# Kernel optimization log

Measured on AMD Instinct MI355X. Metric: run time of the kernel, lower is better.

## Reference

```python
import jax, jax.numpy as jnp
import numpy as np

EPS = 1e-4  # clamp from module default (0.0001, 1 - 0.0001)


def setup_inputs() -> dict:
    key = jax.random.key(0)
    k1, k2, k3 = jax.random.split(key, 3)
    B, T, C, K = 16, 4096, 512, 3
    x = jax.random.normal(k1, (B, T, C), dtype=jnp.float32)
    # logit_alpha initialized as logit of (0.8, 0.9, 0.98) tiled across channels
    init_alphas = jnp.array([0.8, 0.9, 0.98], dtype=jnp.float32)
    logit_alpha = jnp.broadcast_to(
        (jnp.log(init_alphas) - jnp.log1p(-init_alphas))[:, None], (K, C)
    ).astype(jnp.float32)
    # add small noise so gradients are non-degenerate
    logit_alpha = logit_alpha + 0.01 * jax.random.normal(k2, (K, C), dtype=jnp.float32)
    mix_logits = 0.1 * jax.random.normal(k3, (C, K), dtype=jnp.float32)
    return {"x": x, "logit_alpha": logit_alpha, "mix_logits": mix_logits}


def reference(x, logit_alpha, mix_logits):
    # x: [B,T,C]; logit_alpha: [K,C]; mix_logits: [C,K]
    B, T, C = x.shape
    K = logit_alpha.shape[0]
    a = jnp.clip(jax.nn.sigmoid(logit_alpha), EPS, 1.0 - EPS)  # [K,C]
    b = 1.0 - a

    y0 = jnp.broadcast_to(x[:, 0, None, :], (B, K, C))  # t=0: y = x0 for all K

    def step(y_prev, xt):
        # y_prev: [B,K,C], xt: [B,C]
        y = a * y_prev + b * xt[:, None, :]
        return y, y

    xs = jnp.swapaxes(x[:, 1:, :], 0, 1)  # [T-1,B,C]
    _, ys = jax.lax.scan(step, y0, xs)  # [T-1,B,K,C]
    yk = jnp.concatenate([y0[None], ys], axis=0)  # [T,B,K,C]

    mix = jax.nn.softmax(mix_logits, axis=-1)  # [C,K]
    trend = jnp.einsum('tbkc,ck->tbc', yk, mix)  # [T,B,C]
    return jnp.swapaxes(trend, 0, 1)  # [B,T,C]
```

## Files before the change

### kernel.cpp

```cpp
#include <hip/hip_runtime.h>

#define DEV_INLINE __device__ __forceinline__

constexpr int B = 16, T = 4096, C = 512, K = 3;
constexpr int NC = 64;
constexpr int L  = T / NC;
constexpr int C4 = C / 4;
constexpr float EPS = 1e-4f;


typedef float f4v __attribute__((ext_vector_type(4)));

DEV_INLINE float4 f4mul(float4 a, float4 b) {
  return make_float4(a.x * b.x, a.y * b.y, a.z * b.z, a.w * b.w);
}
DEV_INLINE float4 f4add(float4 a, float4 b) {
  return make_float4(a.x + b.x, a.y + b.y, a.z + b.z, a.w + b.w);
}
DEV_INLINE float4 f4fma(float4 a, float4 b, float4 c) {
  return make_float4(fmaf(a.x, b.x, c.x), fmaf(a.y, b.y, c.y),
                     fmaf(a.z, b.z, c.z), fmaf(a.w, b.w, c.w));
}
DEV_INLINE float4 f4onesub(float4 a) {
  return make_float4(1.f - a.x, 1.f - a.y, 1.f - a.z, 1.f - a.w);
}

DEV_INLINE float sig_clamp(float v) {
  float a = 1.0f / (1.0f + __expf(-v));
  return fminf(fmaxf(a, EPS), 1.0f - EPS);
}
DEV_INLINE float4 sig4(float4 v) {
  return make_float4(sig_clamp(v.x), sig_clamp(v.y), sig_clamp(v.z), sig_clamp(v.w));
}

DEV_INLINE void sm3(float l0, float l1, float l2, float& o0, float& o1, float& o2) {
  float mx = fmaxf(l0, fmaxf(l1, l2));
  float e0 = __expf(l0 - mx), e1 = __expf(l1 - mx), e2 = __expf(l2 - mx);
  float inv = 1.0f / (e0 + e1 + e2);
  o0 = e0 * inv; o1 = e1 * inv; o2 = e2 * inv;
}

DEV_INLINE float4 nt_load(const float4* p) {
  f4v t = __builtin_nontemporal_load(reinterpret_cast<const f4v*>(p));
  float4 r; r.x = t.x; r.y = t.y; r.z = t.z; r.w = t.w; return r;
}

DEV_INLINE void mix4(const float* __restrict__ mix_logits, int c4,
                     float4& m0, float4& m1, float4& m2) {
  const float4* ml = (const float4*)mix_logits;
  const float4 q0 = ml[3 * c4 + 0];
  const float4 q1 = ml[3 * c4 + 1];
  const float4 q2 = ml[3 * c4 + 2];
  sm3(q0.x, q0.y, q0.z, m0.x, m1.x, m2.x);
  sm3(q0.w, q1.x, q1.y, m0.y, m1.y, m2.y);
  sm3(q1.z, q1.w, q2.x, m0.z, m1.z, m2.z);
  sm3(q2.y, q2.z, q2.w, m0.w, m1.w, m2.w);
}

__global__ __launch_bounds__(128) void ema_k1(const float* __restrict__ x,
                                              const float* __restrict__ logit_alpha,
                                              const float* __restrict__ mix_logits,
                                              float* __restrict__ carry_f,
                                              float* __restrict__ out) {
  const int c4 = threadIdx.x;
  const int bi = blockIdx.x;
  const int i  = bi & (NC - 1);

  const float4* la = (const float4*)logit_alpha;
  const float4 a0 = sig4(la[0 * C4 + c4]);
  const float4 a1 = sig4(la[1 * C4 + c4]);
  const float4 a2 = sig4(la[2 * C4 + c4]);
  const float4 b0 = f4onesub(a0), b1 = f4onesub(a1), b2 = f4onesub(a2);

  float4 m0, m1, m2;
  mix4(mix_logits, c4, m0, m1, m2);

  const float4* xb = (const float4*)x + (size_t)bi * L * C4 + c4;
  float4*       ob = (float4*)out     + (size_t)bi * L * C4 + c4;

  float4 y0, y1, y2;
  int jstart;
  if (i == 0) {
    float4 x0 = nt_load(&xb[0]);
    y0 = x0; y1 = x0; y2 = x0;
    ob[0] = f4fma(m0, y0, f4fma(m1, y1, f4mul(m2, y2)));
    jstart = 1;
  } else {
    y0 = make_float4(0.f, 0.f, 0.f, 0.f);
    y1 = y0; y2 = y0;
    jstart = 0;
  }

  #pragma unroll 4
  for (int j = jstart; j < L; ++j) {
    float4 xv = nt_load(&xb[(size_t)j * C4]);
    y0 = f4fma(a0, y0, f4mul(b0, xv));
    y1 = f4fma(a1, y1, f4mul(b1, xv));
    y2 = f4fma(a2, y2, f4mul(b2, xv));
    ob[(size_t)j * C4] = f4fma(m0, y0, f4fma(m1, y1, f4mul(m2, y2)));
  }

  float4* carry = (float4*)carry_f;
  const size_t cb = (size_t)bi * (K * C4) + c4;
  carry[cb + 0 * C4] = y0;
  carry[cb + 1 * C4] = y1;
  carry[cb + 2 * C4] = y2;
}

__global__ __launch_bounds__(128) void ema_k2(const float* __restrict__ logit_alpha,
                                              const float* __restrict__ mix_logits,
                                              const float* __restrict__ carry_f,
                                              float* __restrict__ out) {
  const int c4  = threadIdx.x;
  const int blk = blockIdx.x;
  const int b   = blk / (NC - 1);
  const int i   = blk - b * (NC - 1) + 1;

  const float4* la = (const float4*)logit_alpha;
  const float4 a0 = sig4(la[0 * C4 + c4]);
  const float4 a1 = sig4(la[1 * C4 + c4]);
  const float4 a2 = sig4(la[2 * C4 + c4]);

  float4 m0, m1, m2;
  mix4(mix_logits, c4, m0, m1, m2);

  float4 A0 = a0, A1 = a1, A2 = a2;
  #pragma unroll
  for (int s = 0; s < 6; ++s) { A0 = f4mul(A0, A0); A1 = f4mul(A1, A1); A2 = f4mul(A2, A2); }

  const size_t stride = (size_t)K * C4;
  const float4* cb = (const float4*)carry_f + (size_t)b * NC * stride + c4;
  float4 E0 = cb[0 * C4];
  float4 E1 = cb[1 * C4];
  float4 E2 = cb[2 * C4];
  #pragma unroll 4
  for (int j = 1; j < i; ++j) {
    const float4* cj = cb + (size_t)j * stride;
    E0 = f4fma(A0, E0, cj[0 * C4]);
    E1 = f4fma(A1, E1, cj[1 * C4]);
    E2 = f4fma(A2, E2, cj[2 * C4]);
  }

  const float4 g0 = f4mul(m0, E0);
  const float4 g1 = f4mul(m1, E1);
  const float4 g2 = f4mul(m2, E2);
  float4 p0 = a0, p1 = a1, p2 = a2;

  float4* ob = (float4*)out + (size_t)(b * NC + i) * L * C4 + c4;

  #pragma unroll 4
  for (int j = 0; j < L; ++j) {
    float4 corr = f4fma(p0, g0, f4fma(p1, g1, f4mul(p2, g2)));
    float4 o = ob[(size_t)j * C4];
    ob[(size_t)j * C4] = f4add(o, corr);
    p0 = f4mul(p0, a0);
    p1 = f4mul(p1, a1);
    p2 = f4mul(p2, a2);
  }
}

extern "C" void kernel_launch(void* const* d_in, const int* in_sizes, int n_in,
                              void* d_out, int out_size, void* d_ws, size_t ws_size,
                              hipStream_t stream) {
  const float* x           = (const float*)d_in[0];
  const float* logit_alpha = (const float*)d_in[1];
  const float* mix_logits  = (const float*)d_in[2];
  float* out = (float*)d_out;
  float* ws  = (float*)d_ws;

  ema_k1<<<B * NC, 128, 0, stream>>>(x, logit_alpha, mix_logits, ws, out);
  ema_k2<<<B * (NC - 1), 128, 0, stream>>>(logit_alpha, mix_logits, ws, out);
}
```

Before: 273.3 us.

## Fuse chunk scan and carry correction into one cooperative kernel with grid sync

Merges the two-pass chunked EMA scan into a single cooperative kernel launch that uses a grid-wide barrier between writing chunk carries and applying the cross-chunk correction. Each block keeps its decayed alpha and mix weights in registers across the barrier, so they are not recomputed. The aim is to remove the second kernel launch and its setup. The cost is a grid sync over 1024 blocks, and the cooperative launch requires all blocks to be co-resident. The output tile is still re-read from global memory in the correction pass.

```diff
diff --git a/kernel.cpp b/kernel.cpp
--- a/kernel.cpp
+++ b/kernel.cpp
@@ -1,4 +1,7 @@
 #include <hip/hip_runtime.h>
+#include <hip/hip_cooperative_groups.h>
+
+namespace cg = cooperative_groups;
 
 #define DEV_INLINE __device__ __forceinline__
 
@@ -45,26 +48,15 @@
   float4 r; r.x = t.x; r.y = t.y; r.z = t.z; r.w = t.w; return r;
 }
 
-DEV_INLINE void mix4(const float* __restrict__ mix_logits, int c4,
-                     float4& m0, float4& m1, float4& m2) {
-  const float4* ml = (const float4*)mix_logits;
-  const float4 q0 = ml[3 * c4 + 0];
-  const float4 q1 = ml[3 * c4 + 1];
-  const float4 q2 = ml[3 * c4 + 2];
-  sm3(q0.x, q0.y, q0.z, m0.x, m1.x, m2.x);
-  sm3(q0.w, q1.x, q1.y, m0.y, m1.y, m2.y);
-  sm3(q1.z, q1.w, q2.x, m0.z, m1.z, m2.z);
-  sm3(q2.y, q2.z, q2.w, m0.w, m1.w, m2.w);
-}
-
-__global__ __launch_bounds__(128) void ema_k1(const float* __restrict__ x,
-                                              const float* __restrict__ logit_alpha,
-                                              const float* __restrict__ mix_logits,
-                                              float* __restrict__ carry_f,
-                                              float* __restrict__ out) {
+__global__ __launch_bounds__(128) void ema_fused(const float* __restrict__ x,
+                                                 const float* __restrict__ logit_alpha,
+                                                 const float* __restrict__ mix_logits,
+                                                 float* __restrict__ carry_f,
+                                                 float* __restrict__ out) {
   const int c4 = threadIdx.x;
   const int bi = blockIdx.x;
   const int i  = bi & (NC - 1);
+  const int b  = bi >> 6;
 
   const float4* la = (const float4*)logit_alpha;
   const float4 a0 = sig4(la[0 * C4 + c4]);
@@ -72,8 +64,15 @@
   const float4 a2 = sig4(la[2 * C4 + c4]);
   const float4 b0 = f4onesub(a0), b1 = f4onesub(a1), b2 = f4onesub(a2);
 
+  const float4* ml = (const float4*)mix_logits;
+  const float4 q0 = ml[3 * c4 + 0];
+  const float4 q1 = ml[3 * c4 + 1];
+  const float4 q2 = ml[3 * c4 + 2];
   float4 m0, m1, m2;
-  mix4(mix_logits, c4, m0, m1, m2);
+  sm3(q0.x, q0.y, q0.z, m0.x, m1.x, m2.x);
+  sm3(q0.w, q1.x, q1.y, m0.y, m1.y, m2.y);
+  sm3(q1.z, q1.w, q2.x, m0.z, m1.z, m2.z);
+  sm3(q2.y, q2.z, q2.w, m0.w, m1.w, m2.w);
 
   const float4* xb = (const float4*)x + (size_t)bi * L * C4 + c4;
   float4*       ob = (float4*)out     + (size_t)bi * L * C4 + c4;
@@ -100,42 +99,30 @@
     ob[(size_t)j * C4] = f4fma(m0, y0, f4fma(m1, y1, f4mul(m2, y2)));
   }
 
-  float4* carry = (float4*)carry_f;
-  const size_t cb = (size_t)bi * (K * C4) + c4;
-  carry[cb + 0 * C4] = y0;
-  carry[cb + 1 * C4] = y1;
-  carry[cb + 2 * C4] = y2;
-}
+  {
+    float4* carry = (float4*)carry_f;
+    const size_t cb = (size_t)bi * (K * C4) + c4;
+    carry[cb + 0 * C4] = y0;
+    carry[cb + 1 * C4] = y1;
+    carry[cb + 2 * C4] = y2;
+  }
 
-__global__ __launch_bounds__(128) void ema_k2(const float* __restrict__ logit_alpha,
-                                              const float* __restrict__ mix_logits,
-                                              const float* __restrict__ carry_f,
-                                              float* __restrict__ out) {
-  const int c4  = threadIdx.x;
-  const int blk = blockIdx.x;
-  const int b   = blk / (NC - 1);
-  const int i   = blk - b * (NC - 1) + 1;
+  cg::this_grid().sync();
 
-  const float4* la = (const float4*)logit_alpha;
-  const float4 a0 = sig4(la[0 * C4 + c4]);
-  const float4 a1 = sig4(la[1 * C4 + c4]);
-  const float4 a2 = sig4(la[2 * C4 + c4]);
-
-  float4 m0, m1, m2;
-  mix4(mix_logits, c4, m0, m1, m2);
+  if (i == 0) return;
 
   float4 A0 = a0, A1 = a1, A2 = a2;
   #pragma unroll
   for (int s = 0; s < 6; ++s) { A0 = f4mul(A0, A0); A1 = f4mul(A1, A1); A2 = f4mul(A2, A2); }
 
   const size_t stride = (size_t)K * C4;
-  const float4* cb = (const float4*)carry_f + (size_t)b * NC * stride + c4;
-  float4 E0 = cb[0 * C4];
-  float4 E1 = cb[1 * C4];
-  float4 E2 = cb[2 * C4];
+  const float4* cbp = (const float4*)carry_f + (size_t)b * NC * stride + c4;
+  float4 E0 = cbp[0 * C4];
+  float4 E1 = cbp[1 * C4];
+  float4 E2 = cbp[2 * C4];
   #pragma unroll 4
   for (int j = 1; j < i; ++j) {
-    const float4* cj = cb + (size_t)j * stride;
+    const float4* cj = cbp + (size_t)j * stride;
     E0 = f4fma(A0, E0, cj[0 * C4]);
     E1 = f4fma(A1, E1, cj[1 * C4]);
     E2 = f4fma(A2, E2, cj[2 * C4]);
@@ -145,8 +132,6 @@
   const float4 g1 = f4mul(m1, E1);
   const float4 g2 = f4mul(m2, E2);
   float4 p0 = a0, p1 = a1, p2 = a2;
-
-  float4* ob = (float4*)out + (size_t)(b * NC + i) * L * C4 + c4;
 
   #pragma unroll 4
   for (int j = 0; j < L; ++j) {
@@ -168,6 +153,8 @@
   float* out = (float*)d_out;
   float* ws  = (float*)d_ws;
 
-  ema_k1<<<B * NC, 128, 0, stream>>>(x, logit_alpha, mix_logits, ws, out);
-  ema_k2<<<B * (NC - 1), 128, 0, stream>>>(logit_alpha, mix_logits, ws, out);
+  void* args[] = {(void*)&x, (void*)&logit_alpha, (void*)&mix_logits,
+                  (void*)&ws, (void*)&out};
+  hipLaunchCooperativeKernel((const void*)ema_fused, dim3(B * NC), dim3(128),
+                             args, 0, stream);
 }
```

Result: slower. 396.7 us (+45.1%).
